# Kernel optimization log

Measured on AMD Instinct MI355X. Metric: run time of the kernel, lower is better.

The kernel has to match this reference:

```python
import jax, jax.numpy as jnp
import numpy as np

L, E, D = 4, 512, 256   # layers, model dim (=2*D bidirectional), per-direction hidden
T, B = 100, 1000
EPS = 1e-5

def _layernorm(x, g, b):
    m = x.mean(-1, keepdims=True)
    v = x.var(-1, keepdims=True)
    return (x - m) / jnp.sqrt(v + EPS) * g + b

def _dir_scan(U, vf, vr, bf, br):
    # U: (T, B, 4, D) pre-projected gates; SRU elementwise recurrence over time.
    def step(c, u):
        f = jax.nn.sigmoid(u[:, 1] + vf * c + bf)
        c2 = f * c + (1.0 - f) * u[:, 0]
        r = jax.nn.sigmoid(u[:, 2] + vr * c2 + br)
        h = r * c2 + (1.0 - r) * u[:, 3]   # highway with projected residual u3
        return c2, h
    c0 = jnp.zeros((U.shape[1], U.shape[-1]), U.dtype)
    _, H = jax.lax.scan(step, c0, U)
    return H

def setup_inputs() -> dict:
    key = jax.random.key(0)
    ks = jax.random.split(key, 6)
    return {
        "sentence": jax.random.normal(ks[0], (T, B, E), jnp.float32),
        "sru_W": jax.random.normal(ks[1], (L, 2, E, 4 * D), jnp.float32) / np.float32(np.sqrt(E)),
        "sru_v": jax.random.normal(ks[2], (L, 2, 2, D), jnp.float32) * 0.05,
        "sru_b": jnp.zeros((L, 2, 2, D), jnp.float32),
        "ln_g": jnp.ones((L, E), jnp.float32),
        "ln_b": jnp.zeros((L, E), jnp.float32),
        "W1": jax.random.normal(ks[3], (E, E), jnp.float32) / np.float32(np.sqrt(E)),
        "b1": jnp.zeros((E,), jnp.float32),
        "bn_g": jnp.ones((E,), jnp.float32),
        "bn_b": jnp.zeros((E,), jnp.float32),
        "bn_mean": jnp.zeros((E,), jnp.float32),
        "bn_var": jnp.ones((E,), jnp.float32),
        "W2": jax.random.normal(ks[4], (E, 4), jnp.float32) / np.float32(np.sqrt(E)),
        "b2": jnp.zeros((4,), jnp.float32),
    }

def reference(sentence, sru_W, sru_v, sru_b, ln_g, ln_b, W1, b1, bn_g, bn_b, bn_mean, bn_var, W2, b2):
    x = sentence  # (T, B, E)
    for l in range(L):
        xl = _layernorm(x, ln_g[l], ln_b[l])
        # batched projection for both directions: (2, T, B, 4, D)
        U = jnp.einsum('tbi,dik->dtbk', xl, sru_W[l]).reshape(2, T, B, 4, D)
        Hf = _dir_scan(U[0], sru_v[l, 0, 0], sru_v[l, 0, 1], sru_b[l, 0, 0], sru_b[l, 0, 1])
        Hb = _dir_scan(U[1][::-1], sru_v[l, 1, 0], sru_v[l, 1, 1], sru_b[l, 1, 0], sru_b[l, 1, 1])[::-1]
        x = jnp.concatenate([Hf, Hb], axis=-1)  # (T, B, E)
    # head on flattened tokens (eval mode: dropout off, BN uses running stats)
    h = x.reshape(-1, E) @ W1 + b1
    h = (h - bn_mean) / jnp.sqrt(bn_var + EPS) * bn_g + bn_b
    h = jax.nn.relu(h)
    logits = h @ W2 + b2  # (T*B, 4)
    return jax.nn.log_softmax(logits, axis=-1)
```

## Files before the change

kernel.cpp:

```cpp
#include <hip/hip_runtime.h>
#include <stdint.h>

#define T_DIM 100
#define B_DIM 1000
#define E_DIM 512
#define D_DIM 256
#define L_DIM 4
#define M_TOK (T_DIM * B_DIM)
#define M_PAD 100096
#define K_DIM 512

typedef unsigned short u16;
typedef __bf16 bf16x8 __attribute__((ext_vector_type(8)));
typedef float f32x4 __attribute__((ext_vector_type(4)));
typedef unsigned short ushort8 __attribute__((ext_vector_type(8)));

__device__ __forceinline__ u16 f2bf(float f) {
  unsigned int u = __builtin_bit_cast(unsigned int, f);
  u += 0x7fffu + ((u >> 16) & 1u);
  return (u16)(u >> 16);
}
__device__ __forceinline__ float bf2f(u16 h) {
  unsigned int u = ((unsigned int)h) << 16;
  return __builtin_bit_cast(float, u);
}

__device__ __forceinline__ void gld16(const u16* g, u16* l) {
  __builtin_amdgcn_global_load_lds(
      (const __attribute__((address_space(1))) unsigned int*)g,
      (__attribute__((address_space(3))) unsigned int*)l, 16, 0, 0);
}

__global__ void transpose_cast(const float* __restrict__ in, u16* __restrict__ out,
                               int R, int C) {
  __shared__ float t[32][33];
  const int s = blockIdx.z;
  const float* ib = in + (size_t)s * R * C;
  u16* ob = out + (size_t)s * R * C;
  const int c0 = blockIdx.x * 32, r0 = blockIdx.y * 32;
  const int tx = threadIdx.x, ty = threadIdx.y;
#pragma unroll
  for (int j = 0; j < 4; ++j)
    t[ty + j * 8][tx] = ib[(size_t)(r0 + ty + j * 8) * C + c0 + tx];
  __syncthreads();
#pragma unroll
  for (int j = 0; j < 4; ++j)
    ob[(size_t)(c0 + ty + j * 8) * R + r0 + tx] = f2bf(t[tx][ty + j * 8]);
}

__global__ __launch_bounds__(256) void zero_pad(u16* __restrict__ xl) {
  const int i = blockIdx.x * 256 + threadIdx.x;
  ushort8 z = {0, 0, 0, 0, 0, 0, 0, 0};
  *(ushort8*)(xl + (size_t)M_TOK * 512 + (size_t)i * 8) = z;
}

template <typename TI>
__global__ __launch_bounds__(256) void ln_cast_kernel(
    const TI* __restrict__ x, const float* __restrict__ g,
    const float* __restrict__ b, u16* __restrict__ out) {
  const int wid = threadIdx.x >> 6, lane = threadIdx.x & 63;
  const int row = blockIdx.x * 4 + wid;
  float xe[8];
  if constexpr (sizeof(TI) == 4) {
    const float* xr = (const float*)x + (size_t)row * E_DIM + lane * 8;
    const float4 a = *(const float4*)xr;
    const float4 c = *(const float4*)(xr + 4);
    xe[0] = a.x; xe[1] = a.y; xe[2] = a.z; xe[3] = a.w;
    xe[4] = c.x; xe[5] = c.y; xe[6] = c.z; xe[7] = c.w;
  } else {
    const u16* xr = (const u16*)x + (size_t)row * E_DIM + lane * 8;
    const ushort8 hv = *(const ushort8*)xr;
#pragma unroll
    for (int u = 0; u < 8; ++u) xe[u] = bf2f(hv[u]);
  }
  float s = 0.f, q = 0.f;
#pragma unroll
  for (int u = 0; u < 8; ++u) { s += xe[u]; q += xe[u] * xe[u]; }
#pragma unroll
  for (int off = 32; off; off >>= 1) {
    s += __shfl_xor(s, off, 64);
    q += __shfl_xor(q, off, 64);
  }
  const float mean = s * (1.0f / 512.0f);
  const float var = q * (1.0f / 512.0f) - mean * mean;
  const float rstd = rsqrtf(var + 1e-5f);
  const float4 g0 = *(const float4*)(g + lane * 8);
  const float4 g1 = *(const float4*)(g + lane * 8 + 4);
  const float4 b0 = *(const float4*)(b + lane * 8);
  const float4 b1v = *(const float4*)(b + lane * 8 + 4);
  float ge[8] = {g0.x, g0.y, g0.z, g0.w, g1.x, g1.y, g1.z, g1.w};
  float be[8] = {b0.x, b0.y, b0.z, b0.w, b1v.x, b1v.y, b1v.z, b1v.w};
  ushort8 o;
#pragma unroll
  for (int u = 0; u < 8; ++u)
    o[u] = f2bf((xe[u] - mean) * rstd * ge[u] + be[u]);
  *(ushort8*)(out + (size_t)row * E_DIM + lane * 8) = o;
}

__global__ __launch_bounds__(256, 4) void gemm_bf16(
    const u16* __restrict__ A, const u16* __restrict__ B, u16* __restrict__ C,
    int N, int ntil_shift) {
  __shared__ u16 As[128 * 32];
  __shared__ u16 Bs[128 * 32];
  const int tid = threadIdx.x;
  const int wave = tid >> 6, lane = tid & 63;
  const int wm = wave >> 1, wn = wave & 1;
  const int nz = blockIdx.x;
  const int z = nz >> ntil_shift;
  const int n0 = (nz & ((1 << ntil_shift) - 1)) << 7;
  const size_t m0 = (size_t)blockIdx.y * 128;

  const int c_ld = (lane & 3) ^ ((lane >> 3) & 3);
  const u16* Ag = A + (m0 + wave * 32 + (lane >> 2)) * K_DIM + c_ld * 8;
  const u16* Bg = B + ((size_t)z * N + n0 + wave * 32 + (lane >> 2)) * K_DIM +
                  c_ld * 8;
  u16* Al = As + wave * 1024;
  u16* Bl = Bs + wave * 1024;

  f32x4 acc[4][4] = {};
  const int rA = lane & 15;
  const int ch = lane >> 4;
  const int sw = (ch ^ ((rA >> 1) & 3)) * 8;

  for (int kt = 0; kt < K_DIM; kt += 32) {
    gld16(Ag + kt, Al);
    gld16(Ag + kt + 16 * K_DIM, Al + 512);
    gld16(Bg + kt, Bl);
    gld16(Bg + kt + 16 * K_DIM, Bl + 512);
    __syncthreads();

    bf16x8 af[4], bfr[4];
#pragma unroll
    for (int mi = 0; mi < 4; ++mi)
      af[mi] = *(const bf16x8*)&As[(wm * 64 + mi * 16 + rA) * 32 + sw];
#pragma unroll
    for (int ni = 0; ni < 4; ++ni)
      bfr[ni] = *(const bf16x8*)&Bs[(wn * 64 + ni * 16 + rA) * 32 + sw];
#pragma unroll
    for (int mi = 0; mi < 4; ++mi)
#pragma unroll
      for (int ni = 0; ni < 4; ++ni)
        acc[mi][ni] = __builtin_amdgcn_mfma_f32_16x16x32_bf16(
            af[mi], bfr[ni], acc[mi][ni], 0, 0, 0);
    __syncthreads();
  }

  u16* Cb = C + (size_t)z * M_PAD * N;
  const int rr = (lane >> 4) * 4;
  const int cc = lane & 15;
#pragma unroll
  for (int mi = 0; mi < 4; ++mi) {
#pragma unroll
    for (int ni = 0; ni < 4; ++ni) {
      const size_t row = m0 + wm * 64 + mi * 16 + rr;
      const int col = n0 + wn * 64 + ni * 16 + cc;
#pragma unroll
      for (int r = 0; r < 4; ++r)
        Cb[(row + r) * N + col] = f2bf(acc[mi][ni][r]);
    }
  }
}

__global__ __launch_bounds__(256) void sru_scan(const u16* __restrict__ U,
                                                const float* __restrict__ v,
                                                const float* __restrict__ bb,
                                                u16* __restrict__ xout) {
  const int d = threadIdx.x;
  const int b = blockIdx.x;
  const int dir = blockIdx.y;
  const float vf = v[(dir * 2 + 0) * 256 + d];
  const float vr = v[(dir * 2 + 1) * 256 + d];
  const float bf = bb[(dir * 2 + 0) * 256 + d];
  const float br = bb[(dir * 2 + 1) * 256 + d];
  const u16* Ud = U + (size_t)dir * M_PAD * 1024;
  float c = 0.f;
  for (int s = 0; s < T_DIM; ++s) {
    const int t = dir ? (T_DIM - 1 - s) : s;
    const size_t base = ((size_t)t * B_DIM + b) * 1024 + d;
    const float u0 = bf2f(Ud[base]);
    const float u1 = bf2f(Ud[base + 256]);
    const float u2 = bf2f(Ud[base + 512]);
    const float u3 = bf2f(Ud[base + 768]);
    const float f = 1.f / (1.f + __expf(-(u1 + vf * c + bf)));
    c = f * c + (1.f - f) * u0;
    const float r = 1.f / (1.f + __expf(-(u2 + vr * c + br)));
    const float h = r * c + (1.f - r) * u3;
    xout[((size_t)t * B_DIM + b) * 512 + dir * 256 + d] = f2bf(h);
  }
}

__global__ __launch_bounds__(256) void head_kernel(
    const u16* __restrict__ h, const float* __restrict__ b1,
    const float* __restrict__ bn_g, const float* __restrict__ bn_b,
    const float* __restrict__ bn_mean, const float* __restrict__ bn_var,
    const float* __restrict__ W2, const float* __restrict__ b2,
    float* __restrict__ out) {
  const int wid = threadIdx.x >> 6, lane = threadIdx.x & 63;
  const int row = blockIdx.x * 4 + wid;
  const u16* hr = h + (size_t)row * E_DIM + lane * 8;
  const ushort8 hv = *(const ushort8*)hr;
  float s0 = 0.f, s1 = 0.f, s2 = 0.f, s3 = 0.f;
  const int j0 = lane * 8;
#pragma unroll
  for (int u = 0; u < 8; ++u) {
    const int j = j0 + u;
    const float hb = bf2f(hv[u]) + b1[j];
    float hn = (hb - bn_mean[j]) * rsqrtf(bn_var[j] + 1e-5f) * bn_g[j] + bn_b[j];
    hn = fmaxf(hn, 0.f);
    const float4 w = *(const float4*)(W2 + j * 4);
    s0 += hn * w.x; s1 += hn * w.y; s2 += hn * w.z; s3 += hn * w.w;
  }
#pragma unroll
  for (int off = 32; off; off >>= 1) {
    s0 += __shfl_xor(s0, off, 64);
    s1 += __shfl_xor(s1, off, 64);
    s2 += __shfl_xor(s2, off, 64);
    s3 += __shfl_xor(s3, off, 64);
  }
  if (lane == 0) {
    const float4 bv = *(const float4*)b2;
    const float l0 = s0 + bv.x, l1 = s1 + bv.y, l2 = s2 + bv.z, l3 = s3 + bv.w;
    const float mx = fmaxf(fmaxf(l0, l1), fmaxf(l2, l3));
    const float lse =
        mx + logf(__expf(l0 - mx) + __expf(l1 - mx) + __expf(l2 - mx) + __expf(l3 - mx));
    float4 o = {l0 - lse, l1 - lse, l2 - lse, l3 - lse};
    *(float4*)(out + (size_t)row * 4) = o;
  }
}

extern "C" void kernel_launch(void* const* d_in, const int* in_sizes, int n_in,
                              void* d_out, int out_size, void* d_ws, size_t ws_size,
                              hipStream_t stream) {
  const float* sentence = (const float*)d_in[0];
  const float* sru_W = (const float*)d_in[1];
  const float* sru_v = (const float*)d_in[2];
  const float* sru_b = (const float*)d_in[3];
  const float* ln_g = (const float*)d_in[4];
  const float* ln_b = (const float*)d_in[5];
  const float* W1 = (const float*)d_in[6];
  const float* b1 = (const float*)d_in[7];
  const float* bn_g = (const float*)d_in[8];
  const float* bn_b = (const float*)d_in[9];
  const float* bn_mean = (const float*)d_in[10];
  const float* bn_var = (const float*)d_in[11];
  const float* W2 = (const float*)d_in[12];
  const float* b2 = (const float*)d_in[13];

  char* ws = (char*)d_ws;
  const size_t XL_OFF = 0;
  const size_t X_OFF = XL_OFF + (size_t)M_PAD * 512 * 2;
  const size_t U_OFF = X_OFF + (size_t)M_TOK * 512 * 2;
  const size_t WT_OFF = U_OFF + (size_t)2 * M_PAD * 1024 * 2;
  const size_t W1T_OFF = WT_OFF + (size_t)8 * 512 * 1024 * 2;
  u16* xl = (u16*)(ws + XL_OFF);
  u16* x_buf = (u16*)(ws + X_OFF);
  u16* U = (u16*)(ws + U_OFF);
  u16* WT = (u16*)(ws + WT_OFF);
  u16* W1T = (u16*)(ws + W1T_OFF);
  u16* hbuf = U;

  transpose_cast<<<dim3(32, 16, 8), dim3(32, 8), 0, stream>>>(sru_W, WT, 512, 1024);
  transpose_cast<<<dim3(16, 16, 1), dim3(32, 8), 0, stream>>>(W1, W1T, 512, 512);
  zero_pad<<<24, 256, 0, stream>>>(xl);

  for (int l = 0; l < L_DIM; ++l) {
    if (l == 0)
      ln_cast_kernel<float><<<M_TOK / 4, 256, 0, stream>>>(
          sentence, ln_g, ln_b, xl);
    else
      ln_cast_kernel<u16><<<M_TOK / 4, 256, 0, stream>>>(
          x_buf, ln_g + l * 512, ln_b + l * 512, xl);
    gemm_bf16<<<dim3(16, M_PAD / 128), 256, 0, stream>>>(
        xl, WT + (size_t)l * 2 * 1024 * 512, U, 1024, 3);
    u16* xo = (l == L_DIM - 1) ? xl : x_buf;
    sru_scan<<<dim3(1000, 2), 256, 0, stream>>>(U, sru_v + l * 1024,
                                                sru_b + l * 1024, xo);
  }
  gemm_bf16<<<dim3(4, M_PAD / 128), 256, 0, stream>>>(xl, W1T, hbuf, 512, 2);
  head_kernel<<<M_TOK / 4, 256, 0, stream>>>(hbuf, b1, bn_g, bn_b, bn_mean,
                                             bn_var, W2, b2, (float*)d_out);
}
```

Baseline: 2.200 ms.

## Replace GEMM with 256x256-tile, 4-stage pipelined, XCD-aware bf16 MFMA kernel

Replaces the 128x128 single-buffered GEMM with a 512-thread 256x256 tile kernel. It uses a 4-deep LDS ring, prefetching three K-steps ahead with explicit vmcnt waits, and raises wave priority around the MFMA blocks. Block indices are remapped so that M-tiles are grouped per XCD, for L2 locality of the A rows shared across N-tiles. The aim is to hide global-load latency and raise arithmetic intensity, at the cost of more LDS (64KB) and registers, which may limit occupancy. It also relies on hand-tuned waitcnt counts.

```diff
diff --git a/kernel.cpp b/kernel.cpp
--- a/kernel.cpp
+++ b/kernel.cpp
@@ -9,6 +9,7 @@
 #define M_TOK (T_DIM * B_DIM)
 #define M_PAD 100096
 #define K_DIM 512
+#define MT_NUM (M_PAD / 256)
 
 typedef unsigned short u16;
 typedef __bf16 bf16x8 __attribute__((ext_vector_type(8)));
@@ -97,68 +98,107 @@
   *(ushort8*)(out + (size_t)row * E_DIM + lane * 8) = o;
 }
 
-__global__ __launch_bounds__(256, 4) void gemm_bf16(
+__global__ __launch_bounds__(512, 2) void gemm256(
     const u16* __restrict__ A, const u16* __restrict__ B, u16* __restrict__ C,
-    int N, int ntil_shift) {
-  __shared__ u16 As[128 * 32];
-  __shared__ u16 Bs[128 * 32];
+    int N, int nc_shift, int ncol_shift) {
+  __shared__ u16 As[4][8192];
+  __shared__ u16 Bs[4][8192];
+
+  const int bid = blockIdx.x;
+  const int xcd = bid & 7;
+  const int kk = bid >> 3;
+  const int cix = kk & ((1 << nc_shift) - 1);
+  const int jj = kk >> nc_shift;
+  const int mt = xcd + 8 * jj;
+  if (mt >= MT_NUM) return;
+  const int z = cix >> ncol_shift;
+  const int n0 = (cix & ((1 << ncol_shift) - 1)) << 8;
+
   const int tid = threadIdx.x;
   const int wave = tid >> 6, lane = tid & 63;
-  const int wm = wave >> 1, wn = wave & 1;
-  const int nz = blockIdx.x;
-  const int z = nz >> ntil_shift;
-  const int n0 = (nz & ((1 << ntil_shift) - 1)) << 7;
-  const size_t m0 = (size_t)blockIdx.y * 128;
-
+  const int wm = wave >> 2, wn = wave & 3;
+
+  const int r_l = lane >> 2;
   const int c_ld = (lane & 3) ^ ((lane >> 3) & 3);
-  const u16* Ag = A + (m0 + wave * 32 + (lane >> 2)) * K_DIM + c_ld * 8;
-  const u16* Bg = B + ((size_t)z * N + n0 + wave * 32 + (lane >> 2)) * K_DIM +
-                  c_ld * 8;
-  u16* Al = As + wave * 1024;
-  u16* Bl = Bs + wave * 1024;
-
-  f32x4 acc[4][4] = {};
+  const u16* Ag = A + ((size_t)mt * 256 + wave * 32 + r_l) * K_DIM + c_ld * 8;
+  const u16* Bg = B + ((size_t)z * N + n0 + wave * 32 + r_l) * K_DIM + c_ld * 8;
+
+  auto STAGE = [&](int t) {
+    u16* al = &As[t & 3][wave * 1024];
+    u16* bl = &Bs[t & 3][wave * 1024];
+    const u16* ag = Ag + t * 32;
+    const u16* bg = Bg + t * 32;
+    gld16(ag, al);
+    gld16(ag + 16 * K_DIM, al + 512);
+    gld16(bg, bl);
+    gld16(bg + 16 * K_DIM, bl + 512);
+  };
+
+  STAGE(0);
+  STAGE(1);
+  STAGE(2);
+
+  f32x4 acc[8][4] = {};
   const int rA = lane & 15;
-  const int ch = lane >> 4;
-  const int sw = (ch ^ ((rA >> 1) & 3)) * 8;
-
-  for (int kt = 0; kt < K_DIM; kt += 32) {
-    gld16(Ag + kt, Al);
-    gld16(Ag + kt + 16 * K_DIM, Al + 512);
-    gld16(Bg + kt, Bl);
-    gld16(Bg + kt + 16 * K_DIM, Bl + 512);
-    __syncthreads();
-
-    bf16x8 af[4], bfr[4];
-#pragma unroll
-    for (int mi = 0; mi < 4; ++mi)
-      af[mi] = *(const bf16x8*)&As[(wm * 64 + mi * 16 + rA) * 32 + sw];
-#pragma unroll
-    for (int ni = 0; ni < 4; ++ni)
-      bfr[ni] = *(const bf16x8*)&Bs[(wn * 64 + ni * 16 + rA) * 32 + sw];
-#pragma unroll
-    for (int mi = 0; mi < 4; ++mi)
-#pragma unroll
-      for (int ni = 0; ni < 4; ++ni)
-        acc[mi][ni] = __builtin_amdgcn_mfma_f32_16x16x32_bf16(
-            af[mi], bfr[ni], acc[mi][ni], 0, 0, 0);
-    __syncthreads();
+  const int sw = ((lane >> 4) ^ ((rA >> 1) & 3)) * 8;
+  const int offA = (wm * 128 + rA) * 32 + sw;
+  const int offB = (wn * 64 + rA) * 32 + sw;
+
+#pragma unroll
+  for (int t = 0; t < 16; ++t) {
+    if (t < 14)
+      asm volatile("s_waitcnt vmcnt(8) lgkmcnt(0)" ::: "memory");
+    else if (t == 14)
+      asm volatile("s_waitcnt vmcnt(4) lgkmcnt(0)" ::: "memory");
+    else
+      asm volatile("s_waitcnt vmcnt(0) lgkmcnt(0)" ::: "memory");
+    __builtin_amdgcn_s_barrier();
+    asm volatile("" ::: "memory");
+
+    const u16* Ab = As[t & 3];
+    const u16* Bb = Bs[t & 3];
+    bf16x8 bfr[4], af[4];
+#pragma unroll
+    for (int fn = 0; fn < 4; ++fn)
+      bfr[fn] = *(const bf16x8*)&Bb[offB + fn * 512];
+#pragma unroll
+    for (int fm = 0; fm < 4; ++fm)
+      af[fm] = *(const bf16x8*)&Ab[offA + fm * 512];
+    if (t + 3 < 16) STAGE(t + 3);
+    __builtin_amdgcn_s_setprio(1);
+#pragma unroll
+    for (int fm = 0; fm < 4; ++fm)
+#pragma unroll
+      for (int fn = 0; fn < 4; ++fn)
+        acc[fm][fn] = __builtin_amdgcn_mfma_f32_16x16x32_bf16(
+            af[fm], bfr[fn], acc[fm][fn], 0, 0, 0);
+    __builtin_amdgcn_s_setprio(0);
+#pragma unroll
+    for (int fm = 0; fm < 4; ++fm)
+      af[fm] = *(const bf16x8*)&Ab[offA + (fm + 4) * 512];
+    __builtin_amdgcn_s_setprio(1);
+#pragma unroll
+    for (int fm = 0; fm < 4; ++fm)
+#pragma unroll
+      for (int fn = 0; fn < 4; ++fn)
+        acc[fm + 4][fn] = __builtin_amdgcn_mfma_f32_16x16x32_bf16(
+            af[fm], bfr[fn], acc[fm + 4][fn], 0, 0, 0);
+    __builtin_amdgcn_s_setprio(0);
   }
 
   u16* Cb = C + (size_t)z * M_PAD * N;
   const int rr = (lane >> 4) * 4;
   const int cc = lane & 15;
 #pragma unroll
-  for (int mi = 0; mi < 4; ++mi) {
-#pragma unroll
-    for (int ni = 0; ni < 4; ++ni) {
-      const size_t row = m0 + wm * 64 + mi * 16 + rr;
-      const int col = n0 + wn * 64 + ni * 16 + cc;
+  for (int fm = 0; fm < 8; ++fm)
+#pragma unroll
+    for (int fn = 0; fn < 4; ++fn) {
+      const size_t row = (size_t)mt * 256 + wm * 128 + fm * 16 + rr;
+      const int col = n0 + wn * 64 + fn * 16 + cc;
 #pragma unroll
       for (int r = 0; r < 4; ++r)
-        Cb[(row + r) * N + col] = f2bf(acc[mi][ni][r]);
+        Cb[(row + r) * N + col] = f2bf(acc[fm][fn][r]);
     }
-  }
 }
 
 __global__ __launch_bounds__(256) void sru_scan(const u16* __restrict__ U,
@@ -270,13 +310,13 @@
     else
       ln_cast_kernel<u16><<<M_TOK / 4, 256, 0, stream>>>(
           x_buf, ln_g + l * 512, ln_b + l * 512, xl);
-    gemm_bf16<<<dim3(16, M_PAD / 128), 256, 0, stream>>>(
-        xl, WT + (size_t)l * 2 * 1024 * 512, U, 1024, 3);
+    gemm256<<<dim3(8 * 8 * 49), 512, 0, stream>>>(
+        xl, WT + (size_t)l * 2 * 1024 * 512, U, 1024, 3, 2);
     u16* xo = (l == L_DIM - 1) ? xl : x_buf;
     sru_scan<<<dim3(1000, 2), 256, 0, stream>>>(U, sru_v + l * 1024,
                                                 sru_b + l * 1024, xo);
   }
-  gemm_bf16<<<dim3(4, M_PAD / 128), 256, 0, stream>>>(xl, W1T, hbuf, 512, 2);
+  gemm256<<<dim3(8 * 2 * 49), 512, 0, stream>>>(xl, W1T, hbuf, 512, 1, 1);
   head_kernel<<<M_TOK / 4, 256, 0, stream>>>(hbuf, b1, bn_g, bn_b, bn_mean,
                                              bn_var, W2, b2, (float*)d_out);
 }
```

New measurement: 2.308 ms. 1.05x slower.

## Double-buffer GEMM LDS, remap blocks per XCD, interleave gate columns for scan

Applied to the files above, without the earlier changes.

The GEMM now double-buffers its LDS tiles so the next K-slice's global-to-LDS load is issued before the current slice's MFMAs, with one barrier per iteration instead of two. It also uses a 1D grid that assigns M-tiles by XCD index to improve L2 reuse of the A rows. The SRU weight transpose permutes output columns so each hidden unit's four gates sit next to each other, letting the scan read them with one 8-byte load instead of four strided 2-byte loads. The costs are doubled LDS use, which may reduce occupancy, and the C writes now land in an interleaved layout.

```diff
diff --git a/kernel.cpp b/kernel.cpp
--- a/kernel.cpp
+++ b/kernel.cpp
@@ -9,11 +9,13 @@
 #define M_TOK (T_DIM * B_DIM)
 #define M_PAD 100096
 #define K_DIM 512
+#define MT128 782
 
 typedef unsigned short u16;
 typedef __bf16 bf16x8 __attribute__((ext_vector_type(8)));
 typedef float f32x4 __attribute__((ext_vector_type(4)));
 typedef unsigned short ushort8 __attribute__((ext_vector_type(8)));
+typedef unsigned short ushort4v __attribute__((ext_vector_type(4)));
 
 __device__ __forceinline__ u16 f2bf(float f) {
   unsigned int u = __builtin_bit_cast(unsigned int, f);
@@ -32,7 +34,7 @@
 }
 
 __global__ void transpose_cast(const float* __restrict__ in, u16* __restrict__ out,
-                               int R, int C) {
+                               int R, int C, int perm4) {
   __shared__ float t[32][33];
   const int s = blockIdx.z;
   const float* ib = in + (size_t)s * R * C;
@@ -44,8 +46,11 @@
     t[ty + j * 8][tx] = ib[(size_t)(r0 + ty + j * 8) * C + c0 + tx];
   __syncthreads();
 #pragma unroll
-  for (int j = 0; j < 4; ++j)
-    ob[(size_t)(c0 + ty + j * 8) * R + r0 + tx] = f2bf(t[tx][ty + j * 8]);
+  for (int j = 0; j < 4; ++j) {
+    const int cc = c0 + ty + j * 8;
+    const int n = perm4 ? ((cc & 255) * 4 + (cc >> 8)) : cc;
+    ob[(size_t)n * R + r0 + tx] = f2bf(t[tx][ty + j * 8]);
+  }
 }
 
 __global__ __launch_bounds__(256) void zero_pad(u16* __restrict__ xl) {
@@ -99,50 +104,74 @@
 
 __global__ __launch_bounds__(256, 4) void gemm_bf16(
     const u16* __restrict__ A, const u16* __restrict__ B, u16* __restrict__ C,
-    int N, int ntil_shift) {
-  __shared__ u16 As[128 * 32];
-  __shared__ u16 Bs[128 * 32];
+    int N, int nc_shift, int ncol_shift) {
+  __shared__ u16 As[2][4096];
+  __shared__ u16 Bs[2][4096];
+
+  const int bid = blockIdx.x;
+  const int xcd = bid & 7;
+  const int kk = bid >> 3;
+  const int cix = kk & ((1 << nc_shift) - 1);
+  const int jj = kk >> nc_shift;
+  const int mt = xcd + 8 * jj;
+  if (mt >= MT128) return;
+  const int z = cix >> ncol_shift;
+  const int n0 = (cix & ((1 << ncol_shift) - 1)) << 7;
+
   const int tid = threadIdx.x;
   const int wave = tid >> 6, lane = tid & 63;
   const int wm = wave >> 1, wn = wave & 1;
-  const int nz = blockIdx.x;
-  const int z = nz >> ntil_shift;
-  const int n0 = (nz & ((1 << ntil_shift) - 1)) << 7;
-  const size_t m0 = (size_t)blockIdx.y * 128;
-
+
+  const int r_l = lane >> 2;
   const int c_ld = (lane & 3) ^ ((lane >> 3) & 3);
-  const u16* Ag = A + (m0 + wave * 32 + (lane >> 2)) * K_DIM + c_ld * 8;
-  const u16* Bg = B + ((size_t)z * N + n0 + wave * 32 + (lane >> 2)) * K_DIM +
-                  c_ld * 8;
-  u16* Al = As + wave * 1024;
-  u16* Bl = Bs + wave * 1024;
+  const u16* Ag = A + ((size_t)mt * 128 + wave * 32 + r_l) * K_DIM + c_ld * 8;
+  const u16* Bg = B + ((size_t)z * N + n0 + wave * 32 + r_l) * K_DIM + c_ld * 8;
+
+  auto STAGE = [&](int t) {
+    u16* al = &As[t & 1][wave * 1024];
+    u16* bl = &Bs[t & 1][wave * 1024];
+    const u16* ag = Ag + t * 32;
+    const u16* bg = Bg + t * 32;
+    gld16(ag, al);
+    gld16(ag + 16 * K_DIM, al + 512);
+    gld16(bg, bl);
+    gld16(bg + 16 * K_DIM, bl + 512);
+  };
+
+  STAGE(0);
 
   f32x4 acc[4][4] = {};
   const int rA = lane & 15;
-  const int ch = lane >> 4;
-  const int sw = (ch ^ ((rA >> 1) & 3)) * 8;
-
-  for (int kt = 0; kt < K_DIM; kt += 32) {
-    gld16(Ag + kt, Al);
-    gld16(Ag + kt + 16 * K_DIM, Al + 512);
-    gld16(Bg + kt, Bl);
-    gld16(Bg + kt + 16 * K_DIM, Bl + 512);
-    __syncthreads();
-
+  const int sw = ((lane >> 4) ^ ((rA >> 1) & 3)) * 8;
+  const int offA = (wm * 64 + rA) * 32 + sw;
+  const int offB = (wn * 64 + rA) * 32 + sw;
+
+  asm volatile("s_waitcnt vmcnt(0)" ::: "memory");
+  asm volatile("s_barrier" ::: "memory");
+
+#pragma unroll
+  for (int t = 0; t < 16; ++t) {
+    if (t < 15) STAGE(t + 1);
+    const u16* Ab = As[t & 1];
+    const u16* Bb = Bs[t & 1];
     bf16x8 af[4], bfr[4];
 #pragma unroll
     for (int mi = 0; mi < 4; ++mi)
-      af[mi] = *(const bf16x8*)&As[(wm * 64 + mi * 16 + rA) * 32 + sw];
+      af[mi] = *(const bf16x8*)&Ab[offA + mi * 512];
 #pragma unroll
     for (int ni = 0; ni < 4; ++ni)
-      bfr[ni] = *(const bf16x8*)&Bs[(wn * 64 + ni * 16 + rA) * 32 + sw];
+      bfr[ni] = *(const bf16x8*)&Bs[t & 1][offB + ni * 512];
 #pragma unroll
     for (int mi = 0; mi < 4; ++mi)
 #pragma unroll
       for (int ni = 0; ni < 4; ++ni)
         acc[mi][ni] = __builtin_amdgcn_mfma_f32_16x16x32_bf16(
             af[mi], bfr[ni], acc[mi][ni], 0, 0, 0);
-    __syncthreads();
+    (void)Bb;
+    if (t < 15) {
+      asm volatile("s_waitcnt vmcnt(0)" ::: "memory");
+      asm volatile("s_barrier" ::: "memory");
+    }
   }
 
   u16* Cb = C + (size_t)z * M_PAD * N;
@@ -152,7 +181,7 @@
   for (int mi = 0; mi < 4; ++mi) {
 #pragma unroll
     for (int ni = 0; ni < 4; ++ni) {
-      const size_t row = m0 + wm * 64 + mi * 16 + rr;
+      const size_t row = (size_t)mt * 128 + wm * 64 + mi * 16 + rr;
       const int col = n0 + wn * 64 + ni * 16 + cc;
 #pragma unroll
       for (int r = 0; r < 4; ++r)
@@ -176,11 +205,12 @@
   float c = 0.f;
   for (int s = 0; s < T_DIM; ++s) {
     const int t = dir ? (T_DIM - 1 - s) : s;
-    const size_t base = ((size_t)t * B_DIM + b) * 1024 + d;
-    const float u0 = bf2f(Ud[base]);
-    const float u1 = bf2f(Ud[base + 256]);
-    const float u2 = bf2f(Ud[base + 512]);
-    const float u3 = bf2f(Ud[base + 768]);
+    const size_t base = ((size_t)t * B_DIM + b) * 1024 + d * 4;
+    const ushort4v uv = *(const ushort4v*)(Ud + base);
+    const float u0 = bf2f(uv.x);
+    const float u1 = bf2f(uv.y);
+    const float u2 = bf2f(uv.z);
+    const float u3 = bf2f(uv.w);
     const float f = 1.f / (1.f + __expf(-(u1 + vf * c + bf)));
     c = f * c + (1.f - f) * u0;
     const float r = 1.f / (1.f + __expf(-(u2 + vr * c + br)));
@@ -259,8 +289,8 @@
   u16* W1T = (u16*)(ws + W1T_OFF);
   u16* hbuf = U;
 
-  transpose_cast<<<dim3(32, 16, 8), dim3(32, 8), 0, stream>>>(sru_W, WT, 512, 1024);
-  transpose_cast<<<dim3(16, 16, 1), dim3(32, 8), 0, stream>>>(W1, W1T, 512, 512);
+  transpose_cast<<<dim3(32, 16, 8), dim3(32, 8), 0, stream>>>(sru_W, WT, 512, 1024, 1);
+  transpose_cast<<<dim3(16, 16, 1), dim3(32, 8), 0, stream>>>(W1, W1T, 512, 512, 0);
   zero_pad<<<24, 256, 0, stream>>>(xl);
 
   for (int l = 0; l < L_DIM; ++l) {
@@ -270,13 +300,13 @@
     else
       ln_cast_kernel<u16><<<M_TOK / 4, 256, 0, stream>>>(
           x_buf, ln_g + l * 512, ln_b + l * 512, xl);
-    gemm_bf16<<<dim3(16, M_PAD / 128), 256, 0, stream>>>(
-        xl, WT + (size_t)l * 2 * 1024 * 512, U, 1024, 3);
+    gemm_bf16<<<dim3(8 * 16 * 98), 256, 0, stream>>>(
+        xl, WT + (size_t)l * 2 * 1024 * 512, U, 1024, 4, 3);
     u16* xo = (l == L_DIM - 1) ? xl : x_buf;
     sru_scan<<<dim3(1000, 2), 256, 0, stream>>>(U, sru_v + l * 1024,
                                                 sru_b + l * 1024, xo);
   }
-  gemm_bf16<<<dim3(4, M_PAD / 128), 256, 0, stream>>>(xl, W1T, hbuf, 512, 2);
+  gemm_bf16<<<dim3(8 * 4 * 98), 256, 0, stream>>>(xl, W1T, hbuf, 512, 2, 2);
   head_kernel<<<M_TOK / 4, 256, 0, stream>>>(hbuf, b1, bn_g, bn_b, bn_mean,
                                              bn_var, W2, b2, (float*)d_out);
 }
```

New measurement: 2.174 ms. Within noise of the previous version (-1.2%).
